# Kernel tuning notes

Hardware: AMD Instinct MI355X
Metric: run time of the kernel (lower is better)

The kernel has to match this reference:

```python
import jax, jax.numpy as jnp
import numpy as np
import math

# Module hyperparameters (match init_kwargs)
T_FRAMES = 12
LEN_Q = 8160          # sum_l H_l*W_l for levels (64,96),(32,48),(16,24),(8,12)
D_MODEL = 256
N_HEADS = 8
N_LEVELS = 4
T_WINDOW = 2
N_CURR = 4            # n_curr_points
N_TEMP = 2            # n_temporal_points
D_HEAD = D_MODEL // N_HEADS


def _offset_biases():
    """Replicates _reset_parameters() grid init for the offset biases."""
    thetas = np.arange(N_HEADS, dtype=np.float32) * (2.0 * math.pi / N_HEADS)
    grid = np.stack([np.cos(thetas), np.sin(thetas)], -1)            # (H, 2)
    grid = grid / np.abs(grid).max(-1, keepdims=True)
    curr = np.tile(grid.reshape(N_HEADS, 1, 1, 2), (1, N_LEVELS, N_CURR, 1))
    curr = curr * (np.arange(1, N_CURR + 1, dtype=np.float32).reshape(1, 1, N_CURR, 1))
    temp = np.tile(grid.reshape(N_HEADS, 1, 1, 1, 2), (1, N_LEVELS, T_WINDOW, N_TEMP, 1))
    temp = temp * (np.arange(1, N_TEMP + 1, dtype=np.float32).reshape(1, 1, 1, N_TEMP, 1))
    return jnp.asarray(curr.reshape(-1)), jnp.asarray(temp.reshape(-1))


def setup_inputs() -> dict:
    key = jax.random.key(0)
    ks = jax.random.split(key, 10)
    s = 0.02
    b_so, b_tso = _offset_biases()
    d_so = N_HEADS * N_LEVELS * N_CURR * 2          # 256
    d_aw = N_HEADS * N_LEVELS * N_CURR              # 128
    d_tso = N_HEADS * N_LEVELS * T_WINDOW * N_TEMP * 2  # 512
    d_taw = N_HEADS * N_LEVELS * T_WINDOW * N_TEMP      # 256
    return {
        "query": jax.random.normal(ks[0], (T_FRAMES, LEN_Q, D_MODEL), jnp.float32),
        "input_flatten": jax.random.normal(ks[1], (T_FRAMES, LEN_Q, D_MODEL), jnp.float32),
        "W_val": jax.random.normal(ks[2], (D_MODEL, D_MODEL), jnp.float32) * s,
        "b_val": jnp.zeros((D_MODEL,), jnp.float32),
        "W_so": jax.random.normal(ks[3], (D_MODEL, d_so), jnp.float32) * s,
        "b_so": b_so,
        "W_aw": jax.random.normal(ks[4], (D_MODEL, d_aw), jnp.float32) * s,
        "b_aw": jnp.zeros((d_aw,), jnp.float32),
        "W_tso": jax.random.normal(ks[5], (D_MODEL, d_tso), jnp.float32) * s,
        "b_tso": b_tso,
        "W_taw": jax.random.normal(ks[6], (D_MODEL, d_taw), jnp.float32) * s,
        "b_taw": jnp.zeros((d_taw,), jnp.float32),
    }


def reference(query, input_flatten, W_val, b_val, W_so, b_so, W_aw, b_aw,
              W_tso, b_tso, W_taw, b_taw):
    T, Lq, _ = query.shape
    # value projection -> (T, Len_in, H, D_head)
    value = (input_flatten @ W_val + b_val).reshape(T, -1, N_HEADS, D_HEAD)
    # current-frame sampling offsets -> (T, Lq, H, L, n_curr, 2)
    curr_off = (query @ W_so + b_so).reshape(T, Lq, N_HEADS, N_LEVELS, N_CURR, 2)
    # temporal sampling offsets -> (T, Lq, H, t_window*L, n_temp, 2) (flatten(3,4))
    temp_off = (query @ W_tso + b_tso).reshape(
        T, Lq, N_HEADS, T_WINDOW, N_LEVELS, N_TEMP, 2
    ).reshape(T, Lq, N_HEADS, T_WINDOW * N_LEVELS, N_TEMP, 2)
    # joint softmax over current + temporal attention logits
    caw = (query @ W_aw + b_aw).reshape(T, Lq, N_HEADS, N_LEVELS * N_CURR)
    taw = (query @ W_taw + b_taw).reshape(T, Lq, N_HEADS, T_WINDOW * N_LEVELS * N_TEMP)
    aw = jax.nn.softmax(jnp.concatenate([caw, taw], axis=-1), axis=-1)
    n_c = N_LEVELS * N_CURR
    aw_curr = aw[..., :n_c].reshape(T, Lq, N_HEADS, N_LEVELS, N_CURR)
    aw_temp = aw[..., n_c:].reshape(T, Lq, N_HEADS, T_WINDOW * N_LEVELS, N_TEMP)
    return (value, curr_off, temp_off, aw_curr, aw_temp)
```

## Files before the change

kernel.cpp:

```cpp
#include <hip/hip_runtime.h>
#include <stdint.h>

#define AS1 __attribute__((address_space(1)))
#define AS3 __attribute__((address_space(3)))

typedef __attribute__((ext_vector_type(8))) short short8;
typedef __attribute__((ext_vector_type(4))) float floatx4;

__device__ __forceinline__ unsigned short f2b_rne(float f) {
  union { float f; unsigned u; } c; c.f = f;
  unsigned u = c.u;
  unsigned r = u + 0x7fffu + ((u >> 16) & 1u);
  return (unsigned short)(r >> 16);
}

__global__ void prep_weights(const float* __restrict__ Wv,  const float* __restrict__ bv,
                             const float* __restrict__ Wso, const float* __restrict__ bso,
                             const float* __restrict__ Waw, const float* __restrict__ baw,
                             const float* __restrict__ Wtso,const float* __restrict__ btso,
                             const float* __restrict__ Wtaw,const float* __restrict__ btaw,
                             unsigned short* __restrict__ Wt, float* __restrict__ bcat) {
  int n = blockIdx.x;
  int k = threadIdx.x;
  const float* W; const float* b; int c, N;
  if (n < 256)      { W = Wv;   b = bv;   c = n;       N = 256; }
  else if (n < 512) { W = Wso;  b = bso;  c = n - 256; N = 256; }
  else if (n < 768) { W = Wtso; b = btso; c = n - 512; N = 256; }
  else if (n < 896) { W = Waw;  b = baw;  c = n - 768; N = 128; }
  else              { W = Wtaw; b = btaw; c = n - 896; N = 128; }
  int c8 = k >> 3, lo = k & 7;
  int cs;
  if (n < 768) cs = (c8 & ~7) | ((c8 ^ n) & 7);
  else         cs = (c8 & ~3) | ((c8 ^ n) & 3);
  Wt[n * 256 + cs * 8 + lo] = f2b_rne(W[(size_t)k * N + c]);
  if (k == 0) bcat[n] = b[c];
}

__global__ __launch_bounds__(256, 3)
void fused_all(const float* __restrict__ Q, const float* __restrict__ X,
               const unsigned short* __restrict__ Wt, const float* __restrict__ bcat,
               float* __restrict__ out, int M) {
  __shared__ __align__(16) char lds[49152];

  const int tid  = threadIdx.x;
  const int lane = tid & 63;
  const int wid  = tid >> 6;
  const int lrow = lane & 15;
  const int quad = lane >> 4;
  const int mw   = (wid >> 1) * 32;
  const int nw   = (wid & 1) * 64;
  const int mBase = blockIdx.x * 64;

  for (int phase = 0; phase < 2; ++phase) {
    const float* A = (phase == 0) ? X : Q;
    {
      float4 va[16];
#pragma unroll
      for (int i = 0; i < 16; ++i) {
        int id = i * 256 + tid;
        int r = id >> 6, c4 = id & 63;
        va[i] = *(const float4*)(A + (size_t)(mBase + r) * 256 + c4 * 4);
      }
#pragma unroll
      for (int i = 0; i < 16; ++i) {
        int id = i * 256 + tid;
        int r = id >> 6, c4 = id & 63;
        int c8 = c4 >> 1, hf = c4 & 1;
        int pos = (c8 & ~7) | ((c8 ^ r) & 7);
        uint2 pk;
        pk.x = ((unsigned)f2b_rne(va[i].y) << 16) | f2b_rne(va[i].x);
        pk.y = ((unsigned)f2b_rne(va[i].w) << 16) | f2b_rne(va[i].z);
        *(uint2*)(lds + r * 512 + pos * 16 + hf * 8) = pk;
      }
    }
    const int ntBeg = phase ? 2 : 0;
    const int ntEnd = phase ? 6 : 2;
    for (int nt = ntBeg; nt < ntEnd; ++nt) {
      const int nBase = nt * 128;
      const unsigned short* Bb = Wt + (size_t)nBase * 256;
      floatx4 acc[2][4] = {};
      for (int s = 0; s < 4; ++s) {
#pragma unroll
        for (int ci = 0; ci < 4; ++ci) {
          int g = ci * 256 + tid;
          int r = g >> 3, j = g & 7;
          const unsigned short* src = Bb + (size_t)r * 256 + s * 64 + j * 8;
          unsigned ldsoff = 32768u + (unsigned)((ci * 256 + (tid & ~63)) * 16);
          __builtin_amdgcn_global_load_lds((const AS1 void*)src,
                                           (AS3 void*)(lds + ldsoff), 16, 0, 0);
        }
        __syncthreads();
        short8 af[2][2], bf[4][2];
#pragma unroll
        for (int mi = 0; mi < 2; ++mi) {
          int row = mw + mi * 16 + lrow;
#pragma unroll
          for (int kk = 0; kk < 2; ++kk) {
            int j = kk * 4 + quad;
            af[mi][kk] = *(const short8*)(lds + row * 512 + (s * 8 + (j ^ (row & 7))) * 16);
          }
        }
#pragma unroll
        for (int ni = 0; ni < 4; ++ni) {
          int r = nw + ni * 16 + lrow;
#pragma unroll
          for (int kk = 0; kk < 2; ++kk) {
            int j = kk * 4 + quad;
            bf[ni][kk] = *(const short8*)(lds + 32768 + r * 128 + ((j ^ (r & 7)) * 16));
          }
        }
#pragma unroll
        for (int kk = 0; kk < 2; ++kk)
#pragma unroll
          for (int mi = 0; mi < 2; ++mi)
#pragma unroll
            for (int ni = 0; ni < 4; ++ni)
              acc[mi][ni] = __builtin_amdgcn_mfma_f32_16x16x32_bf16(
                  bf[ni][kk], af[mi][kk], acc[mi][ni], 0, 0, 0);
        __syncthreads();
      }
      const int seg = nt >> 1, halfn = nt & 1;
      float* O = out + (size_t)seg * ((size_t)M * 256) + halfn * 128;
#pragma unroll
      for (int ni = 0; ni < 4; ++ni) {
        float4 b4 = *(const float4*)(bcat + nBase + nw + ni * 16 + quad * 4);
#pragma unroll
        for (int mi = 0; mi < 2; ++mi) {
          int row = mBase + mw + mi * 16 + lrow;
          float4 v;
          v.x = acc[mi][ni][0] + b4.x;
          v.y = acc[mi][ni][1] + b4.y;
          v.z = acc[mi][ni][2] + b4.z;
          v.w = acc[mi][ni][3] + b4.w;
          *(float4*)(O + (size_t)row * 256 + nw + ni * 16 + quad * 4) = v;
        }
      }
    }
  }

  floatx4 acc2[4][4] = {};
  for (int s = 0; s < 8; ++s) {
#pragma unroll
    for (int ci = 0; ci < 4; ++ci) {
      int g = ci * 64 + lane;
      int sr = g >> 2, j = g & 3;
      int n = (sr < 32) ? (768 + 32 * wid + sr) : (896 + 32 * wid + (sr - 32));
      const unsigned short* src = Wt + (size_t)n * 256 + s * 32 + j * 8;
      unsigned ldsoff = 32768u + (unsigned)(wid * 4096 + ci * 1024);
      __builtin_amdgcn_global_load_lds((const AS1 void*)src,
                                       (AS3 void*)(lds + ldsoff), 16, 0, 0);
    }
    __syncthreads();
    short8 wa[4], qf[4];
#pragma unroll
    for (int t = 0; t < 4; ++t) {
      wa[t] = *(const short8*)(lds + 32768 + wid * 4096 + (t * 16 + lrow) * 64 +
                               (quad ^ (lrow & 3)) * 16);
    }
#pragma unroll
    for (int qt = 0; qt < 4; ++qt) {
      int row = qt * 16 + lrow;
      int cg = s * 4 + quad;
      int pos = (cg & ~7) | ((cg ^ (row & 7)) & 7);
      qf[qt] = *(const short8*)(lds + row * 512 + pos * 16);
    }
#pragma unroll
    for (int qt = 0; qt < 4; ++qt)
#pragma unroll
      for (int t = 0; t < 4; ++t)
        acc2[qt][t] = __builtin_amdgcn_mfma_f32_16x16x32_bf16(
            wa[t], qf[qt], acc2[qt][t], 0, 0, 0);
    __syncthreads();
  }

  float* awc = out + (size_t)3 * ((size_t)M * 256);
  float* awt = awc + (size_t)M * 128;
#pragma unroll
  for (int hp = 0; hp < 2; ++hp) {
    const int h = 2 * wid + hp;
    float4 bc = *(const float4*)(bcat + 768 + h * 16 + quad * 4);
    float4 bt = *(const float4*)(bcat + 896 + h * 16 + quad * 4);
#pragma unroll
    for (int qt = 0; qt < 4; ++qt) {
      float c0 = acc2[qt][hp][0] + bc.x;
      float c1 = acc2[qt][hp][1] + bc.y;
      float c2 = acc2[qt][hp][2] + bc.z;
      float c3 = acc2[qt][hp][3] + bc.w;
      float t0 = acc2[qt][2 + hp][0] + bt.x;
      float t1 = acc2[qt][2 + hp][1] + bt.y;
      float t2 = acc2[qt][2 + hp][2] + bt.z;
      float t3 = acc2[qt][2 + hp][3] + bt.w;
      float mx = fmaxf(fmaxf(fmaxf(c0, c1), fmaxf(c2, c3)),
                       fmaxf(fmaxf(t0, t1), fmaxf(t2, t3)));
      mx = fmaxf(mx, __shfl_xor(mx, 16));
      mx = fmaxf(mx, __shfl_xor(mx, 32));
      float e0 = __expf(c0 - mx), e1 = __expf(c1 - mx);
      float e2 = __expf(c2 - mx), e3 = __expf(c3 - mx);
      float f0 = __expf(t0 - mx), f1 = __expf(t1 - mx);
      float f2 = __expf(t2 - mx), f3 = __expf(t3 - mx);
      float sm = ((e0 + e1) + (e2 + e3)) + ((f0 + f1) + (f2 + f3));
      sm += __shfl_xor(sm, 16);
      sm += __shfl_xor(sm, 32);
      float inv = 1.0f / sm;
      int row = mBase + qt * 16 + lrow;
      float4 oc = make_float4(e0 * inv, e1 * inv, e2 * inv, e3 * inv);
      float4 ot = make_float4(f0 * inv, f1 * inv, f2 * inv, f3 * inv);
      *(float4*)(awc + (size_t)row * 128 + h * 16 + quad * 4) = oc;
      *(float4*)(awt + (size_t)row * 128 + h * 16 + quad * 4) = ot;
    }
  }
}

extern "C" void kernel_launch(void* const* d_in, const int* in_sizes, int n_in,
                              void* d_out, int out_size, void* d_ws, size_t ws_size,
                              hipStream_t stream) {
  const float* Q    = (const float*)d_in[0];
  const float* Xf   = (const float*)d_in[1];
  const float* Wv   = (const float*)d_in[2];
  const float* bv   = (const float*)d_in[3];
  const float* Wso  = (const float*)d_in[4];
  const float* bso  = (const float*)d_in[5];
  const float* Waw  = (const float*)d_in[6];
  const float* baw  = (const float*)d_in[7];
  const float* Wtso = (const float*)d_in[8];
  const float* btso = (const float*)d_in[9];
  const float* Wtaw = (const float*)d_in[10];
  const float* btaw = (const float*)d_in[11];
  float* out = (float*)d_out;

  unsigned short* Wt = (unsigned short*)d_ws;
  float* bcat = (float*)((char*)d_ws + 1024 * 256 * 2);

  int M = in_sizes[0] / 256;

  prep_weights<<<1024, 256, 0, stream>>>(Wv, bv, Wso, bso, Waw, baw,
                                         Wtso, btso, Wtaw, btaw, Wt, bcat);

  fused_all<<<M / 64, 256, 0, stream>>>(Q, Xf, Wt, bcat, out, M);
}
```

Before: 187.2 us.

## Load weight fragments straight from global into registers, drop LDS staging and syncs

Weight tiles are no longer staged through LDS with global_load_lds and barriers. Each wave now reads its B fragments directly from global memory (L2-resident), using an unswizzled weight layout and a double-buffered register prefetch across K steps. LDS shrinks to 32 KB, which may allow more resident blocks. Activation loads and output stores switch to nontemporal hints to avoid cache pollution from streaming data. The tradeoff is redundant per-wave global weight reads and higher register pressure in exchange for fewer barriers and less LDS traffic.

Measured after the change: 272.3 us. 45.5% more time.

```diff
diff --git a/kernel.cpp b/kernel.cpp
--- a/kernel.cpp
+++ b/kernel.cpp
@@ -1,8 +1,5 @@
 #include <hip/hip_runtime.h>
 #include <stdint.h>
-
-#define AS1 __attribute__((address_space(1)))
-#define AS3 __attribute__((address_space(3)))
 
 typedef __attribute__((ext_vector_type(8))) short short8;
 typedef __attribute__((ext_vector_type(4))) float floatx4;
@@ -28,11 +25,7 @@
   else if (n < 768) { W = Wtso; b = btso; c = n - 512; N = 256; }
   else if (n < 896) { W = Waw;  b = baw;  c = n - 768; N = 128; }
   else              { W = Wtaw; b = btaw; c = n - 896; N = 128; }
-  int c8 = k >> 3, lo = k & 7;
-  int cs;
-  if (n < 768) cs = (c8 & ~7) | ((c8 ^ n) & 7);
-  else         cs = (c8 & ~3) | ((c8 ^ n) & 3);
-  Wt[n * 256 + cs * 8 + lo] = f2b_rne(W[(size_t)k * N + c]);
+  Wt[n * 256 + k] = f2b_rne(W[(size_t)k * N + c]);
   if (k == 0) bcat[n] = b[c];
 }
 
@@ -40,7 +33,7 @@
 void fused_all(const float* __restrict__ Q, const float* __restrict__ X,
                const unsigned short* __restrict__ Wt, const float* __restrict__ bcat,
                float* __restrict__ out, int M) {
-  __shared__ __align__(16) char lds[49152];
+  __shared__ __align__(16) char lds[32768];
 
   const int tid  = threadIdx.x;
   const int lane = tid & 63;
@@ -53,13 +46,15 @@
 
   for (int phase = 0; phase < 2; ++phase) {
     const float* A = (phase == 0) ? X : Q;
+    if (phase == 1) __syncthreads();
     {
-      float4 va[16];
+      floatx4 va[16];
 #pragma unroll
       for (int i = 0; i < 16; ++i) {
         int id = i * 256 + tid;
         int r = id >> 6, c4 = id & 63;
-        va[i] = *(const float4*)(A + (size_t)(mBase + r) * 256 + c4 * 4);
+        va[i] = __builtin_nontemporal_load(
+            (const floatx4*)(A + (size_t)(mBase + r) * 256 + c4 * 4));
       }
 #pragma unroll
       for (int i = 0; i < 16; ++i) {
@@ -68,95 +63,78 @@
         int c8 = c4 >> 1, hf = c4 & 1;
         int pos = (c8 & ~7) | ((c8 ^ r) & 7);
         uint2 pk;
-        pk.x = ((unsigned)f2b_rne(va[i].y) << 16) | f2b_rne(va[i].x);
-        pk.y = ((unsigned)f2b_rne(va[i].w) << 16) | f2b_rne(va[i].z);
+        pk.x = ((unsigned)f2b_rne(va[i][1]) << 16) | f2b_rne(va[i][0]);
+        pk.y = ((unsigned)f2b_rne(va[i][3]) << 16) | f2b_rne(va[i][2]);
         *(uint2*)(lds + r * 512 + pos * 16 + hf * 8) = pk;
       }
     }
+    __syncthreads();
+
     const int ntBeg = phase ? 2 : 0;
     const int ntEnd = phase ? 6 : 2;
     for (int nt = ntBeg; nt < ntEnd; ++nt) {
       const int nBase = nt * 128;
-      const unsigned short* Bb = Wt + (size_t)nBase * 256;
+      const unsigned short* Bw = Wt + (size_t)(nBase + nw + lrow) * 256 + quad * 8;
       floatx4 acc[2][4] = {};
-      for (int s = 0; s < 4; ++s) {
-#pragma unroll
-        for (int ci = 0; ci < 4; ++ci) {
-          int g = ci * 256 + tid;
-          int r = g >> 3, j = g & 7;
-          const unsigned short* src = Bb + (size_t)r * 256 + s * 64 + j * 8;
-          unsigned ldsoff = 32768u + (unsigned)((ci * 256 + (tid & ~63)) * 16);
-          __builtin_amdgcn_global_load_lds((const AS1 void*)src,
-                                           (AS3 void*)(lds + ldsoff), 16, 0, 0);
-        }
-        __syncthreads();
-        short8 af[2][2], bf[4][2];
-#pragma unroll
-        for (int mi = 0; mi < 2; ++mi) {
-          int row = mw + mi * 16 + lrow;
-#pragma unroll
-          for (int kk = 0; kk < 2; ++kk) {
-            int j = kk * 4 + quad;
-            af[mi][kk] = *(const short8*)(lds + row * 512 + (s * 8 + (j ^ (row & 7))) * 16);
-          }
-        }
-#pragma unroll
-        for (int ni = 0; ni < 4; ++ni) {
-          int r = nw + ni * 16 + lrow;
-#pragma unroll
-          for (int kk = 0; kk < 2; ++kk) {
-            int j = kk * 4 + quad;
-            bf[ni][kk] = *(const short8*)(lds + 32768 + r * 128 + ((j ^ (r & 7)) * 16));
-          }
-        }
-#pragma unroll
-        for (int kk = 0; kk < 2; ++kk)
-#pragma unroll
-          for (int mi = 0; mi < 2; ++mi)
-#pragma unroll
-            for (int ni = 0; ni < 4; ++ni)
-              acc[mi][ni] = __builtin_amdgcn_mfma_f32_16x16x32_bf16(
-                  bf[ni][kk], af[mi][kk], acc[mi][ni], 0, 0, 0);
-        __syncthreads();
-      }
+      short8 bA[4][2], bB[4][2];
+
+#define LOADB(dst, s_)                                                        \
+  do {                                                                        \
+    _Pragma("unroll") for (int ni = 0; ni < 4; ++ni)                          \
+      _Pragma("unroll") for (int kk = 0; kk < 2; ++kk)                        \
+        dst[ni][kk] = *(const short8*)(Bw + ni * 4096 + (s_) * 64 + kk * 32); \
+  } while (0)
+
+#define COMPUTE(bb, s_)                                                        \
+  do {                                                                         \
+    short8 af[2][2];                                                           \
+    _Pragma("unroll") for (int mi = 0; mi < 2; ++mi) {                         \
+      int row = mw + mi * 16 + lrow;                                           \
+      _Pragma("unroll") for (int kk = 0; kk < 2; ++kk)                         \
+        af[mi][kk] = *(const short8*)(                                         \
+            lds + row * 512 + ((s_) * 8 + ((kk * 4 + quad) ^ (row & 7))) * 16);\
+    }                                                                          \
+    _Pragma("unroll") for (int kk = 0; kk < 2; ++kk)                           \
+      _Pragma("unroll") for (int mi = 0; mi < 2; ++mi)                         \
+        _Pragma("unroll") for (int ni = 0; ni < 4; ++ni)                       \
+          acc[mi][ni] = __builtin_amdgcn_mfma_f32_16x16x32_bf16(               \
+              bb[ni][kk], af[mi][kk], acc[mi][ni], 0, 0, 0);                   \
+  } while (0)
+
+      LOADB(bA, 0);
+      LOADB(bB, 1); COMPUTE(bA, 0);
+      LOADB(bA, 2); COMPUTE(bB, 1);
+      LOADB(bB, 3); COMPUTE(bA, 2);
+      COMPUTE(bB, 3);
+#undef LOADB
+#undef COMPUTE
+
       const int seg = nt >> 1, halfn = nt & 1;
       float* O = out + (size_t)seg * ((size_t)M * 256) + halfn * 128;
 #pragma unroll
       for (int ni = 0; ni < 4; ++ni) {
-        float4 b4 = *(const float4*)(bcat + nBase + nw + ni * 16 + quad * 4);
+        floatx4 b4 = *(const floatx4*)(bcat + nBase + nw + ni * 16 + quad * 4);
 #pragma unroll
         for (int mi = 0; mi < 2; ++mi) {
           int row = mBase + mw + mi * 16 + lrow;
-          float4 v;
-          v.x = acc[mi][ni][0] + b4.x;
-          v.y = acc[mi][ni][1] + b4.y;
-          v.z = acc[mi][ni][2] + b4.z;
-          v.w = acc[mi][ni][3] + b4.w;
-          *(float4*)(O + (size_t)row * 256 + nw + ni * 16 + quad * 4) = v;
+          floatx4 v = acc[mi][ni] + b4;
+          __builtin_nontemporal_store(
+              v, (floatx4*)(O + (size_t)row * 256 + nw + ni * 16 + quad * 4));
         }
       }
     }
   }
 
+  const unsigned short* Wc = Wt + (size_t)(768 + 32 * wid + lrow) * 256 + quad * 8;
+  const unsigned short* Wtp = Wt + (size_t)(896 + 32 * wid + lrow) * 256 + quad * 8;
   floatx4 acc2[4][4] = {};
+#pragma unroll
   for (int s = 0; s < 8; ++s) {
-#pragma unroll
-    for (int ci = 0; ci < 4; ++ci) {
-      int g = ci * 64 + lane;
-      int sr = g >> 2, j = g & 3;
-      int n = (sr < 32) ? (768 + 32 * wid + sr) : (896 + 32 * wid + (sr - 32));
-      const unsigned short* src = Wt + (size_t)n * 256 + s * 32 + j * 8;
-      unsigned ldsoff = 32768u + (unsigned)(wid * 4096 + ci * 1024);
-      __builtin_amdgcn_global_load_lds((const AS1 void*)src,
-                                       (AS3 void*)(lds + ldsoff), 16, 0, 0);
-    }
-    __syncthreads();
     short8 wa[4], qf[4];
-#pragma unroll
-    for (int t = 0; t < 4; ++t) {
-      wa[t] = *(const short8*)(lds + 32768 + wid * 4096 + (t * 16 + lrow) * 64 +
-                               (quad ^ (lrow & 3)) * 16);
-    }
+    wa[0] = *(const short8*)(Wc + s * 32);
+    wa[1] = *(const short8*)(Wc + 16 * 256 + s * 32);
+    wa[2] = *(const short8*)(Wtp + s * 32);
+    wa[3] = *(const short8*)(Wtp + 16 * 256 + s * 32);
 #pragma unroll
     for (int qt = 0; qt < 4; ++qt) {
       int row = qt * 16 + lrow;
@@ -170,7 +148,6 @@
       for (int t = 0; t < 4; ++t)
         acc2[qt][t] = __builtin_amdgcn_mfma_f32_16x16x32_bf16(
             wa[t], qf[qt], acc2[qt][t], 0, 0, 0);
-    __syncthreads();
   }
 
   float* awc = out + (size_t)3 * ((size_t)M * 256);
@@ -178,18 +155,18 @@
 #pragma unroll
   for (int hp = 0; hp < 2; ++hp) {
     const int h = 2 * wid + hp;
-    float4 bc = *(const float4*)(bcat + 768 + h * 16 + quad * 4);
-    float4 bt = *(const float4*)(bcat + 896 + h * 16 + quad * 4);
+    floatx4 bc = *(const floatx4*)(bcat + 768 + h * 16 + quad * 4);
+    floatx4 bt = *(const floatx4*)(bcat + 896 + h * 16 + quad * 4);
 #pragma unroll
     for (int qt = 0; qt < 4; ++qt) {
-      float c0 = acc2[qt][hp][0] + bc.x;
-      float c1 = acc2[qt][hp][1] + bc.y;
-      float c2 = acc2[qt][hp][2] + bc.z;
-      float c3 = acc2[qt][hp][3] + bc.w;
-      float t0 = acc2[qt][2 + hp][0] + bt.x;
-      float t1 = acc2[qt][2 + hp][1] + bt.y;
-      float t2 = acc2[qt][2 + hp][2] + bt.z;
-      float t3 = acc2[qt][2 + hp][3] + bt.w;
+      float c0 = acc2[qt][hp][0] + bc[0];
+      float c1 = acc2[qt][hp][1] + bc[1];
+      float c2 = acc2[qt][hp][2] + bc[2];
+      float c3 = acc2[qt][hp][3] + bc[3];
+      float t0 = acc2[qt][2 + hp][0] + bt[0];
+      float t1 = acc2[qt][2 + hp][1] + bt[1];
+      float t2 = acc2[qt][2 + hp][2] + bt[2];
+      float t3 = acc2[qt][2 + hp][3] + bt[3];
       float mx = fmaxf(fmaxf(fmaxf(c0, c1), fmaxf(c2, c3)),
                        fmaxf(fmaxf(t0, t1), fmaxf(t2, t3)));
       mx = fmaxf(mx, __shfl_xor(mx, 16));
@@ -203,10 +180,10 @@
       sm += __shfl_xor(sm, 32);
       float inv = 1.0f / sm;
       int row = mBase + qt * 16 + lrow;
-      float4 oc = make_float4(e0 * inv, e1 * inv, e2 * inv, e3 * inv);
-      float4 ot = make_float4(f0 * inv, f1 * inv, f2 * inv, f3 * inv);
-      *(float4*)(awc + (size_t)row * 128 + h * 16 + quad * 4) = oc;
-      *(float4*)(awt + (size_t)row * 128 + h * 16 + quad * 4) = ot;
+      floatx4 oc; oc[0] = e0 * inv; oc[1] = e1 * inv; oc[2] = e2 * inv; oc[3] = e3 * inv;
+      floatx4 ot; ot[0] = f0 * inv; ot[1] = f1 * inv; ot[2] = f2 * inv; ot[3] = f3 * inv;
+      __builtin_nontemporal_store(oc, (floatx4*)(awc + (size_t)row * 128 + h * 16 + quad * 4));
+      __builtin_nontemporal_store(ot, (floatx4*)(awt + (size_t)row * 128 + h * 16 + quad * 4));
     }
   }
 }
```
